# Optimization experiments

Measured on AMD Instinct MI355X. Metric: run time of the kernel, lower is better.

## Reference

```python
import jax, jax.numpy as jnp
import numpy as np

C_CONST = 0.0  # polynomial kernel additive constant (init arg c)
D_CONST = 2    # polynomial kernel degree (init arg d)


def setup_inputs() -> dict:
    key = jax.random.key(0)
    k1, k2 = jax.random.split(key)
    input = jax.random.normal(k1, (1, 64, 128, 64), dtype=jnp.float32)
    target = jax.random.normal(k2, (1, 64, 128, 64), dtype=jnp.float32)
    return {"input": input, "target": target}


def reference(input, target):
    ch = input.shape[1]
    hw_input = input.shape[2] * input.shape[3]
    hw_target = target.shape[2] * target.shape[3]
    # Flatten to [hw, c] feature matrices (batch assumed 1, as in the original view(c, -1).T)
    F = input.reshape(ch, -1).T   # [hw_input, c]
    S = target.reshape(ch, -1).T  # [hw_target, c]

    def kernel(A, B):
        # Naive polynomial kernel Gram matrix: (A @ B^T + c)^d
        return (A @ B.T + C_CONST) ** D_CONST

    loss = kernel(F, F) + kernel(S, S) - 2.0 * kernel(F, S)
    return loss.sum() / hw_input / hw_target / (ch ** 2)
```

## Files before the change

### kernel.cpp

```cpp
#include <hip/hip_runtime.h>


#define CH    64
#define KTOT  8192
#define G1    256
#define KPB   32
#define KPW   8
#define NPART 2
#define NP    (G1 * NPART)

#define NORMF 3.637978807091713e-12f

#define RCOL(row, tb) ((tb) ^ ((row) & 56))

__global__ __launch_bounds__(256, 1) void gram_partial(
    const float* __restrict__ in, const float* __restrict__ tg,
    float* __restrict__ ws, float* __restrict__ out)
{
    __shared__ __attribute__((aligned(16))) float ts_in[KPB][CH];
    __shared__ __attribute__((aligned(16))) float ts_tg[KPB][CH];
    __shared__ __attribute__((aligned(16))) float red[2][CH][CH];

    const int t  = threadIdx.x;
    const int k0 = blockIdx.x * KPB;

    if (blockIdx.x == 0 && t == 0) out[0] = 0.f;

    {
        const int lk = (t & 7) << 2;
#pragma unroll
        for (int r = 0; r < 2; ++r) {
            const int lch = (t >> 3) + 32 * r;
            const float4 vi = *(const float4*)(in + lch * KTOT + k0 + lk);
            const float4 vt = *(const float4*)(tg + lch * KTOT + k0 + lk);
            ts_in[lk + 0][lch] = vi.x; ts_in[lk + 1][lch] = vi.y;
            ts_in[lk + 2][lch] = vi.z; ts_in[lk + 3][lch] = vi.w;
            ts_tg[lk + 0][lch] = vt.x; ts_tg[lk + 1][lch] = vt.y;
            ts_tg[lk + 2][lch] = vt.z; ts_tg[lk + 3][lch] = vt.w;
        }
    }
    __syncthreads();

    const int w    = t >> 6;
    const int lane = t & 63;
    const int ta   = (lane >> 3) << 3;
    const int tb   = (lane & 7) << 3;

    float acc[8][8];
#pragma unroll
    for (int i = 0; i < 8; ++i)
#pragma unroll
        for (int j = 0; j < 8; ++j) acc[i][j] = 0.f;

#pragma unroll
    for (int kk = w * KPW; kk < w * KPW + KPW; ++kk) {
        const float4 x0 = *(const float4*)&ts_in[kk][ta];
        const float4 x1 = *(const float4*)&ts_in[kk][ta + 4];
        const float4 y0 = *(const float4*)&ts_in[kk][tb];
        const float4 y1 = *(const float4*)&ts_in[kk][tb + 4];
        const float4 u0 = *(const float4*)&ts_tg[kk][ta];
        const float4 u1 = *(const float4*)&ts_tg[kk][ta + 4];
        const float4 v0 = *(const float4*)&ts_tg[kk][tb];
        const float4 v1 = *(const float4*)&ts_tg[kk][tb + 4];
        const float A[8] = {x0.x, x0.y, x0.z, x0.w, x1.x, x1.y, x1.z, x1.w};
        const float B[8] = {y0.x, y0.y, y0.z, y0.w, y1.x, y1.y, y1.z, y1.w};
        const float C[8] = {u0.x, u0.y, u0.z, u0.w, u1.x, u1.y, u1.z, u1.w};
        const float D[8] = {v0.x, v0.y, v0.z, v0.w, v1.x, v1.y, v1.z, v1.w};
#pragma unroll
        for (int i = 0; i < 8; ++i)
#pragma unroll
            for (int j = 0; j < 8; ++j) {
                acc[i][j] = fmaf(A[i], B[j], acc[i][j]);
                acc[i][j] = fmaf(-C[i], D[j], acc[i][j]);
            }
    }

    if (w >= 2) {
#pragma unroll
        for (int i = 0; i < 8; ++i) {
            const int row = ta + i;
            const int cc  = RCOL(row, tb);
            float4 a, b;
            a.x = acc[i][0]; a.y = acc[i][1]; a.z = acc[i][2]; a.w = acc[i][3];
            b.x = acc[i][4]; b.y = acc[i][5]; b.z = acc[i][6]; b.w = acc[i][7];
            *(float4*)&red[w - 2][row][cc]     = a;
            *(float4*)&red[w - 2][row][cc + 4] = b;
        }
    }
    __syncthreads();
    if (w < 2) {
        float* p = ws + (blockIdx.x * NPART + w) * 4096;
#pragma unroll
        for (int i = 0; i < 8; ++i) {
            const int row = ta + i;
            const int cc  = RCOL(row, tb);
            const float4 r0 = *(const float4*)&red[w][row][cc];
            const float4 r1 = *(const float4*)&red[w][row][cc + 4];
            float4 a, b;
            a.x = acc[i][0] + r0.x; a.y = acc[i][1] + r0.y;
            a.z = acc[i][2] + r0.z; a.w = acc[i][3] + r0.w;
            b.x = acc[i][4] + r1.x; b.y = acc[i][5] + r1.y;
            b.z = acc[i][6] + r1.z; b.w = acc[i][7] + r1.w;
            *(float4*)(p + row * 64 + tb)     = a;
            *(float4*)(p + row * 64 + tb + 4) = b;
        }
    }
}

__global__ __launch_bounds__(256) void reduce_square(
    const float* __restrict__ ws, float* __restrict__ out)
{
    __shared__ float red2[16][16];
    const int t  = threadIdx.x;
    const int el = t & 15;
    const int sl = t >> 4;
    const int e  = (blockIdx.x << 4) + el;

    float s = 0.f;
    const int p0 = sl * (NP / 16);
#pragma unroll
    for (int p = p0; p < p0 + (NP / 16); ++p)
        s += ws[p * 4096 + e];
    red2[sl][el] = s;
    __syncthreads();

    if (t < 64) {
        float sq = 0.f;
        if (t < 16) {
            float tot = 0.f;
#pragma unroll
            for (int i = 0; i < 16; ++i) tot += red2[i][t];
            sq = tot * tot;
        }
#pragma unroll
        for (int off = 8; off > 0; off >>= 1)
            sq += __shfl_down(sq, off);
        if (t == 0) atomicAdd(out, sq * NORMF);
    }
}

extern "C" void kernel_launch(void* const* d_in, const int* in_sizes, int n_in,
                              void* d_out, int out_size, void* d_ws, size_t ws_size,
                              hipStream_t stream)
{
    const float* in = (const float*)d_in[0];
    const float* tg = (const float*)d_in[1];
    float* out = (float*)d_out;
    float* ws  = (float*)d_ws;

    gram_partial<<<G1, 256, 0, stream>>>(in, tg, ws, out);
    reduce_square<<<256, 256, 0, stream>>>(ws, out);
}
```

Before: 69.27 us.

## Fuse Gram partial and reduce-square kernels with an atomic grid barrier

Merges the two launches into one kernel. After computing its Gram-difference tile, each block reduces all four waves' partials in shared memory and writes one 64x64 partial instead of two. Blocks then wait on a software grid barrier built from monotonic atomic counters in the workspace, and each block performs its slice of the cross-block sum and square. This removes the second launch and halves partial-buffer traffic. In exchange, correctness relies on all 256 blocks being co-resident and on the counter area starting at zero.

Result: slower. 90.20 us (+30.2%).

```diff
diff --git a/kernel.cpp b/kernel.cpp
--- a/kernel.cpp
+++ b/kernel.cpp
@@ -6,14 +6,14 @@
 #define G1    256
 #define KPB   32
 #define KPW   8
-#define NPART 2
-#define NP    (G1 * NPART)
 
 #define NORMF 3.637978807091713e-12f
 
+#define PART_FLOATS (G1 * 4096)
+
 #define RCOL(row, tb) ((tb) ^ ((row) & 56))
 
-__global__ __launch_bounds__(256, 1) void gram_partial(
+__global__ __launch_bounds__(256) void fused_loss(
     const float* __restrict__ in, const float* __restrict__ tg,
     float* __restrict__ ws, float* __restrict__ out)
 {
@@ -22,9 +22,10 @@
     __shared__ __attribute__((aligned(16))) float red[2][CH][CH];
 
     const int t  = threadIdx.x;
-    const int k0 = blockIdx.x * KPB;
+    const int b  = blockIdx.x;
+    const int k0 = b * KPB;
 
-    if (blockIdx.x == 0 && t == 0) out[0] = 0.f;
+    if (b == 0 && t == 0) out[0] = 0.f;
 
     {
         const int lk = (t & 7) << 2;
@@ -80,62 +81,106 @@
         for (int i = 0; i < 8; ++i) {
             const int row = ta + i;
             const int cc  = RCOL(row, tb);
-            float4 a, b;
-            a.x = acc[i][0]; a.y = acc[i][1]; a.z = acc[i][2]; a.w = acc[i][3];
-            b.x = acc[i][4]; b.y = acc[i][5]; b.z = acc[i][6]; b.w = acc[i][7];
+            float4 a, bb;
+            a.x  = acc[i][0]; a.y  = acc[i][1]; a.z  = acc[i][2]; a.w  = acc[i][3];
+            bb.x = acc[i][4]; bb.y = acc[i][5]; bb.z = acc[i][6]; bb.w = acc[i][7];
             *(float4*)&red[w - 2][row][cc]     = a;
-            *(float4*)&red[w - 2][row][cc + 4] = b;
+            *(float4*)&red[w - 2][row][cc + 4] = bb;
         }
     }
     __syncthreads();
     if (w < 2) {
-        float* p = ws + (blockIdx.x * NPART + w) * 4096;
 #pragma unroll
         for (int i = 0; i < 8; ++i) {
             const int row = ta + i;
             const int cc  = RCOL(row, tb);
             const float4 r0 = *(const float4*)&red[w][row][cc];
             const float4 r1 = *(const float4*)&red[w][row][cc + 4];
-            float4 a, b;
-            a.x = acc[i][0] + r0.x; a.y = acc[i][1] + r0.y;
-            a.z = acc[i][2] + r0.z; a.w = acc[i][3] + r0.w;
-            b.x = acc[i][4] + r1.x; b.y = acc[i][5] + r1.y;
-            b.z = acc[i][6] + r1.z; b.w = acc[i][7] + r1.w;
-            *(float4*)(p + row * 64 + tb)     = a;
-            *(float4*)(p + row * 64 + tb + 4) = b;
+            acc[i][0] += r0.x; acc[i][1] += r0.y; acc[i][2] += r0.z; acc[i][3] += r0.w;
+            acc[i][4] += r1.x; acc[i][5] += r1.y; acc[i][6] += r1.z; acc[i][7] += r1.w;
         }
     }
-}
-
-__global__ __launch_bounds__(256) void reduce_square(
-    const float* __restrict__ ws, float* __restrict__ out)
-{
-    __shared__ float red2[16][16];
-    const int t  = threadIdx.x;
-    const int el = t & 15;
-    const int sl = t >> 4;
-    const int e  = (blockIdx.x << 4) + el;
-
-    float s = 0.f;
-    const int p0 = sl * (NP / 16);
+    __syncthreads();
+    if (w == 1) {
 #pragma unroll
-    for (int p = p0; p < p0 + (NP / 16); ++p)
-        s += ws[p * 4096 + e];
-    red2[sl][el] = s;
+        for (int i = 0; i < 8; ++i) {
+            const int row = ta + i;
+            const int cc  = RCOL(row, tb);
+            float4 a, bb;
+            a.x  = acc[i][0]; a.y  = acc[i][1]; a.z  = acc[i][2]; a.w  = acc[i][3];
+            bb.x = acc[i][4]; bb.y = acc[i][5]; bb.z = acc[i][6]; bb.w = acc[i][7];
+            *(float4*)&red[0][row][cc]     = a;
+            *(float4*)&red[0][row][cc + 4] = bb;
+        }
+    }
+    __syncthreads();
+    if (w == 0) {
+        float* p = ws + b * 4096;
+#pragma unroll
+        for (int i = 0; i < 8; ++i) {
+            const int row = ta + i;
+            const int cc  = RCOL(row, tb);
+            const float4 r0 = *(const float4*)&red[0][row][cc];
+            const float4 r1 = *(const float4*)&red[0][row][cc + 4];
+            float4 a, bb;
+            a.x  = acc[i][0] + r0.x; a.y  = acc[i][1] + r0.y;
+            a.z  = acc[i][2] + r0.z; a.w  = acc[i][3] + r0.w;
+            bb.x = acc[i][4] + r1.x; bb.y = acc[i][5] + r1.y;
+            bb.z = acc[i][6] + r1.z; bb.w = acc[i][7] + r1.w;
+            *(float4*)(p + row * 64 + tb)     = a;
+            *(float4*)(p + row * 64 + tb + 4) = bb;
+        }
+    }
     __syncthreads();
 
+    {
+        unsigned* ctr = (unsigned*)(ws + PART_FLOATS);
+        unsigned* A   = ctr;
+        unsigned* B   = ctr + 32;
+        if (t == 0) {
+            unsigned S = __hip_atomic_load(B, __ATOMIC_RELAXED,
+                                           __HIP_MEMORY_SCOPE_AGENT);
+            __hip_atomic_fetch_add(A, 1u, __ATOMIC_RELEASE,
+                                   __HIP_MEMORY_SCOPE_AGENT);
+            while (__hip_atomic_load(A, __ATOMIC_ACQUIRE,
+                                     __HIP_MEMORY_SCOPE_AGENT) - S < (unsigned)G1)
+                __builtin_amdgcn_s_sleep(2);
+            __threadfence();
+        }
+        __syncthreads();
+    }
+
+    {
+        const int el = t & 15;
+        const int sl = t >> 4;
+        const int e  = (b << 4) + el;
+        float s = 0.f;
+#pragma unroll
+        for (int p = sl * 16; p < sl * 16 + 16; ++p)
+            s += ws[p * 4096 + e];
+        float* r2 = &red[0][0][0];
+        r2[sl * 16 + el] = s;
+    }
+    __syncthreads();
     if (t < 64) {
+        const float* r2 = &red[0][0][0];
         float sq = 0.f;
         if (t < 16) {
             float tot = 0.f;
 #pragma unroll
-            for (int i = 0; i < 16; ++i) tot += red2[i][t];
+            for (int i = 0; i < 16; ++i) tot += r2[i * 16 + t];
             sq = tot * tot;
         }
 #pragma unroll
         for (int off = 8; off > 0; off >>= 1)
             sq += __shfl_down(sq, off);
         if (t == 0) atomicAdd(out, sq * NORMF);
+    }
+
+    if (t == 0) {
+        unsigned* B = (unsigned*)(ws + PART_FLOATS) + 32;
+        __hip_atomic_fetch_add(B, 1u, __ATOMIC_RELEASE,
+                               __HIP_MEMORY_SCOPE_AGENT);
     }
 }
 
@@ -148,6 +193,5 @@
     float* out = (float*)d_out;
     float* ws  = (float*)d_ws;
 
-    gram_partial<<<G1, 256, 0, stream>>>(in, tg, ws, out);
-    reduce_square<<<256, 256, 0, stream>>>(ws, out);
+    fused_loss<<<G1, 256, 0, stream>>>(in, tg, ws, out);
 }
```
